# Kernel tuning notes

Measured on AMD Instinct MI355X. Metric: run time of the kernel, lower is better.

Reference implementation:

```python
import jax, jax.numpy as jnp
import numpy as np

B, S, T = 512, 1024, 50


def setup_inputs() -> dict:
    key = jax.random.key(0)
    k1, k2, k3, k4, k5, k6, k7 = jax.random.split(key, 7)
    token_scores = jax.random.normal(k1, (B, S, T), dtype=jnp.float32)
    tags = jax.random.randint(k2, (B, S), 0, T, dtype=jnp.int64)
    # left-contiguous mask: each sequence has a random valid length >= 1
    lengths = jax.random.randint(k3, (B,), 1, S + 1)
    token_mask = (jnp.arange(S)[None, :] < lengths[:, None]).astype(jnp.int32)
    transitions = jax.random.normal(k4, (T, T), dtype=jnp.float32) * 0.1
    start_transitions = jax.random.normal(k5, (T,), dtype=jnp.float32) * 0.1
    end_transitions = jax.random.normal(k6, (T,), dtype=jnp.float32) * 0.1
    return {
        "token_scores": token_scores,
        "tags": tags,
        "token_mask": token_mask,
        "transitions": transitions,
        "start_transitions": start_transitions,
        "end_transitions": end_transitions,
    }


def _crf_log_likelihood(token_scores, tags, token_mask, transitions,
                        start_transitions, end_transitions):
    # token_scores: [B,S,T], tags: [B,S] int, token_mask: [B,S] {0,1}
    maskf = token_mask.astype(token_scores.dtype)
    maskb = token_mask.astype(bool)

    # ---- numerator: score of the gold tag path ----
    emit = jnp.take_along_axis(token_scores, tags[..., None], axis=2)[..., 0]  # [B,S]
    emit_sum = jnp.sum(emit * maskf, axis=1)
    trans_sum = jnp.sum(transitions[tags[:, :-1], tags[:, 1:]] * maskf[:, 1:], axis=1)
    start_score = start_transitions[tags[:, 0]]
    last_idx = jnp.sum(token_mask, axis=1).astype(jnp.int32) - 1          # [B]
    last_tags = jnp.take_along_axis(tags, last_idx[:, None], axis=1)[:, 0]
    end_score = end_transitions[last_tags]
    numerator = start_score + emit_sum + trans_sum + end_score            # [B]

    # ---- denominator: log partition via forward algorithm (scan over time) ----
    alpha0 = start_transitions[None, :] + token_scores[:, 0]              # [B,T]
    logits_rest = jnp.swapaxes(token_scores[:, 1:], 0, 1)                 # [S-1,B,T]
    mask_rest = jnp.swapaxes(maskb[:, 1:], 0, 1)                          # [S-1,B]

    def step(alpha, xs):
        logit_t, m_t = xs                                                 # [B,T], [B]
        # inner[b, i, j] = alpha[b,i] + transitions[i,j] + logit_t[b,j]
        inner = alpha[:, :, None] + transitions[None, :, :] + logit_t[:, None, :]
        new_alpha = jax.nn.logsumexp(inner, axis=1)                       # [B,T]
        alpha = jnp.where(m_t[:, None], new_alpha, alpha)
        return alpha, None

    alpha, _ = jax.lax.scan(step, alpha0, (logits_rest, mask_rest))
    denominator = jax.nn.logsumexp(alpha + end_transitions[None, :], axis=1)  # [B]

    return jnp.sum(numerator - denominator)  # scalar, summed over batch


def reference(token_scores, tags, token_mask, transitions,
              start_transitions, end_transitions):
    batch_size = token_scores.shape[0]
    ll = _crf_log_likelihood(token_scores, tags, token_mask, transitions,
                             start_transitions, end_transitions)
    return -ll / float(batch_size)
```

## Files before the change

kernel.cpp:

```cpp
#include <hip/hip_runtime.h>
#include <math.h>

#define CB 512
#define CS 1024
#define CT 50
#define PF 4

__global__ void zero_out_kernel(float* out) { out[0] = 0.0f; }

__device__ __forceinline__ void wave_fence() {
    __builtin_amdgcn_wave_barrier();
    asm volatile("" ::: "memory");
}

__device__ __forceinline__ int lane0_bits(float v) {
    return __builtin_amdgcn_readlane(__float_as_int(v), 0);
}

__global__ __launch_bounds__(128) void crf_scan_kernel(
    const float* __restrict__ scores,
    const int*   __restrict__ tags,
    const int*   __restrict__ mask,
    const float* __restrict__ trans,
    const float* __restrict__ start_tr,
    const float* __restrict__ end_tr,
    float* __restrict__ out)
{
    const int b    = blockIdx.x;
    const int tid  = threadIdx.x;
    const int w    = tid >> 6;
    const int lane = tid & 63;
    const int xl   = (lane < CT) ? lane : 0;

    __shared__ __attribute__((aligned(16))) float sTrans[CT * CT];
    __shared__ __attribute__((aligned(16))) float sP[2][64];
    __shared__ __attribute__((aligned(16))) float sA[64];
    __shared__ __attribute__((aligned(16))) float sB[64];
    __shared__ float sLZ[2], sN[2];

    for (int k = tid; k < CT * CT; k += 128) sTrans[k] = trans[k];
    __syncthreads();

    float ev[CT];
    #pragma unroll
    for (int i = 0; i < CT; ++i)
        ev[i] = __expf((w == 0) ? sTrans[i * CT + xl] : sTrans[xl * CT + i]);

    const int* mrow = mask + (size_t)b * CS;
    int len = 0;
    for (int t = lane; t < CS; t += 64) len += mrow[t];
    #pragma unroll
    for (int off = 32; off; off >>= 1) len += __shfl_xor(len, off);

    const float* srow = scores + (size_t)b * CS * CT;
    const float* sx   = srow + xl;

    const int tm = (len - 1) >> 1;

    const int count = (w == 0) ? tm : ((len >= 2) ? (len - 2 - tm) : 0);
    const int base  = (w == 0) ? 1 : (len - 2);
    const int dir   = (w == 0) ? 1 : -1;

    float st = (w == 0) ? __expf(start_tr[xl] + sx[0])
                        : ((len >= 2) ? __expf(end_tr[xl] + sx[(size_t)(len - 1) * CT])
                                      : __expf(end_tr[xl]));
    int   kexp = 0;
    float* myP = sP[w];

    #define STEP(EXK)                                                       \
    {                                                                       \
        myP[lane] = st;                                                     \
        wave_fence();                                                       \
        float q0 = 0.f, q1 = 0.f, q2 = 0.f, q3 = 0.f;                       \
        _Pragma("unroll")                                                   \
        for (int i = 0; i < 48; i += 4) {                                   \
            const float4 pv = *(const float4*)&myP[i];                      \
            q0 = fmaf(pv.x, ev[i + 0], q0);                                 \
            q1 = fmaf(pv.y, ev[i + 1], q1);                                 \
            q2 = fmaf(pv.z, ev[i + 2], q2);                                 \
            q3 = fmaf(pv.w, ev[i + 3], q3);                                 \
        }                                                                   \
        {                                                                   \
            const float2 pv2 = *(const float2*)&myP[48];                    \
            q0 = fmaf(pv2.x, ev[48], q0);                                   \
            q1 = fmaf(pv2.y, ev[49], q1);                                   \
        }                                                                   \
        wave_fence();                                                       \
        st = ((q0 + q1) + (q2 + q3)) * (EXK);                               \
    }

    #define RENORM()                                                        \
    {                                                                       \
        int sb = lane0_bits(st);                                            \
        int e  = (sb >> 23) & 0xff;                                         \
        kexp  += e - 127;                                                   \
        st    *= __int_as_float((254 - e) << 23);                           \
    }

    float xpf[PF];
    #pragma unroll
    for (int k = 0; k < PF; ++k) {
        int idx = base + dir * k;
        if (idx < 0) idx = 0;
        xpf[k] = sx[(size_t)idx * CT];
    }
    int k = 0;
    while (k + PF <= count) {
        float exk[PF];
        #pragma unroll
        for (int j = 0; j < PF; ++j) exk[j] = __expf(xpf[j]);
        #pragma unroll
        for (int j = 0; j < PF; ++j) {
            int idx = base + dir * (k + PF + j);
            if (idx < 0) idx = 0;
            xpf[j] = sx[(size_t)idx * CT];
        }
        RENORM();
        STEP(exk[0]); STEP(exk[1]); STEP(exk[2]); STEP(exk[3]);
        k += PF;
    }
    for (int r = 0; k < count; ++k, ++r) {
        float exk = __expf(xpf[r]);
        RENORM();
        STEP(exk);
    }

    if (w == 1 && len >= 2) { STEP(1.0f) }
    RENORM();
    #undef STEP
    #undef RENORM

    if (w == 0) sA[lane] = (lane < CT) ? st : 0.0f;
    else        sB[lane] = (lane < CT) ? st : 0.0f;
    if (lane == 0) sLZ[w] = (float)kexp * 0.6931471805599453f;
    __syncthreads();

    const int* trow = tags + (size_t)b * CS;
    float nsum = 0.0f;
    for (int t = tid; t < CS; t += 128) {
        if (t < len) {
            int tg = trow[t];
            nsum += srow[(size_t)t * CT + tg];
            if (t >= 1) nsum += sTrans[trow[t - 1] * CT + tg];
        }
    }
    #pragma unroll
    for (int off = 32; off; off >>= 1) nsum += __shfl_xor(nsum, off);
    if (lane == 0) sN[w] = nsum;

    float den = 0.0f;
    if (w == 0) {
        float vp = sA[lane] * sB[lane];
        #pragma unroll
        for (int off = 32; off; off >>= 1) vp += __shfl_xor(vp, off);
        den = sLZ[0] + sLZ[1] + __logf(vp);
    }
    __syncthreads();

    if (tid == 0) {
        float num = sN[0] + sN[1] + start_tr[trow[0]] + end_tr[trow[len - 1]];
        atomicAdd(out, (den - num) * (1.0f / CB));
    }
}

extern "C" void kernel_launch(void* const* d_in, const int* in_sizes, int n_in,
                              void* d_out, int out_size, void* d_ws, size_t ws_size,
                              hipStream_t stream) {
    const float* scores   = (const float*)d_in[0];
    const int*   tags     = (const int*)d_in[1];
    const int*   mask     = (const int*)d_in[2];
    const float* trans    = (const float*)d_in[3];
    const float* start_tr = (const float*)d_in[4];
    const float* end_tr   = (const float*)d_in[5];
    float* out = (float*)d_out;

    zero_out_kernel<<<1, 1, 0, stream>>>(out);
    crf_scan_kernel<<<CB, 128, 0, stream>>>(scores, tags, mask, trans,
                                            start_tr, end_tr, out);
}
```

Measured before the change: 293.0 us.

## Split the CRF step matvec across lane quads with packed FMA and DPP reduction

Each recurrence step now has every lane compute partial sums for four output tags over a sixteen-state slice of the input. Each lane reads four float4 values from LDS instead of the whole state vector, and uses packed two-wide FMAs. The quad partials are then combined with DPP quad permutes, and each lane picks its own tag's result. This shortens the serial FMA dependency chain and cuts LDS traffic on the latency-bound sequential scan, at the cost of extra permute and select instructions per step. Launch bounds now also declare one block per SIMD minimum.

```diff
diff --git a/kernel.cpp b/kernel.cpp
--- a/kernel.cpp
+++ b/kernel.cpp
@@ -6,6 +6,8 @@
 #define CT 50
 #define PF 4
 
+typedef float v2f __attribute__((ext_vector_type(2)));
+
 __global__ void zero_out_kernel(float* out) { out[0] = 0.0f; }
 
 __device__ __forceinline__ void wave_fence() {
@@ -17,7 +19,13 @@
     return __builtin_amdgcn_readlane(__float_as_int(v), 0);
 }
 
-__global__ __launch_bounds__(128) void crf_scan_kernel(
+template <int CTRL>
+__device__ __forceinline__ float qperm(float v) {
+    return __int_as_float(__builtin_amdgcn_update_dpp(
+        0, __float_as_int(v), CTRL, 0xf, 0xf, false));
+}
+
+__global__ __launch_bounds__(128, 1) void crf_scan_kernel(
     const float* __restrict__ scores,
     const int*   __restrict__ tags,
     const int*   __restrict__ mask,
@@ -31,9 +39,13 @@
     const int w    = tid >> 6;
     const int lane = tid & 63;
     const int xl   = (lane < CT) ? lane : 0;
+    const int g    = lane & 3;
+    const int m    = lane >> 2;
+    const bool selb0 = (lane & 1) != 0;
+    const bool selb1 = (lane & 2) != 0;
 
     __shared__ __attribute__((aligned(16))) float sTrans[CT * CT];
-    __shared__ __attribute__((aligned(16))) float sP[2][64];
+    __shared__ __attribute__((aligned(16))) float sP2[2][64];
     __shared__ __attribute__((aligned(16))) float sA[64];
     __shared__ __attribute__((aligned(16))) float sB[64];
     __shared__ float sLZ[2], sN[2];
@@ -41,10 +53,26 @@
     for (int k = tid; k < CT * CT; k += 128) sTrans[k] = trans[k];
     __syncthreads();
 
-    float ev[CT];
-    #pragma unroll
-    for (int i = 0; i < CT; ++i)
-        ev[i] = __expf((w == 0) ? sTrans[i * CT + xl] : sTrans[xl * CT + i]);
+    v2f EC0[16], EC1[16];
+    {
+        const int i0 = 16 * g, s0 = 4 * m;
+        #pragma unroll
+        for (int k = 0; k < 16; ++k) {
+            const int i = i0 + k;
+            float e[4] = {0.f, 0.f, 0.f, 0.f};
+            if (i < CT) {
+                #pragma unroll
+                for (int c = 0; c < 4; ++c) {
+                    const int s = s0 + c;
+                    if (s < CT)
+                        e[c] = __expf(w == 0 ? sTrans[i * CT + s]
+                                             : sTrans[s * CT + i]);
+                }
+            }
+            EC0[k] = (v2f){e[0], e[1]};
+            EC1[k] = (v2f){e[2], e[3]};
+        }
+    }
 
     const int* mrow = mask + (size_t)b * CS;
     int len = 0;
@@ -55,38 +83,49 @@
     const float* srow = scores + (size_t)b * CS * CT;
     const float* sx   = srow + xl;
 
-    const int tm = (len - 1) >> 1;
-
+    const int tm    = (len - 1) >> 1;
     const int count = (w == 0) ? tm : ((len >= 2) ? (len - 2 - tm) : 0);
     const int base  = (w == 0) ? 1 : (len - 2);
     const int dir   = (w == 0) ? 1 : -1;
 
-    float st = (w == 0) ? __expf(start_tr[xl] + sx[0])
-                        : ((len >= 2) ? __expf(end_tr[xl] + sx[(size_t)(len - 1) * CT])
-                                      : __expf(end_tr[xl]));
-    int   kexp = 0;
-    float* myP = sP[w];
-
-    #define STEP(EXK)                                                       \
+    float st;
+    if (w == 0) {
+        st = (lane < CT) ? __expf(start_tr[lane] + sx[0]) : 0.f;
+    } else {
+        st = (lane < CT)
+            ? ((len >= 2) ? __expf(end_tr[lane] + sx[(size_t)(len - 1) * CT])
+                          : __expf(end_tr[lane]))
+            : 0.f;
+    }
+    int kexp = 0;
+    float* sP = sP2[w];
+    const float* sPq = sP + 16 * g;
+
+    #define STEP(EX)                                                        \
     {                                                                       \
-        myP[lane] = st;                                                     \
+        sP[lane] = st;                                                      \
         wave_fence();                                                       \
-        float q0 = 0.f, q1 = 0.f, q2 = 0.f, q3 = 0.f;                       \
+        const float4 p0 = *(const float4*)&sPq[0];                          \
+        const float4 p1 = *(const float4*)&sPq[4];                          \
+        const float4 p2 = *(const float4*)&sPq[8];                          \
+        const float4 p3 = *(const float4*)&sPq[12];                         \
+        wave_fence();    \
+        float pv[16] = {p0.x,p0.y,p0.z,p0.w, p1.x,p1.y,p1.z,p1.w,           \
+                        p2.x,p2.y,p2.z,p2.w, p3.x,p3.y,p3.z,p3.w};          \
+        v2f a0 = {0.f,0.f}, a1 = {0.f,0.f};                                 \
         _Pragma("unroll")                                                   \
-        for (int i = 0; i < 48; i += 4) {                                   \
-            const float4 pv = *(const float4*)&myP[i];                      \
-            q0 = fmaf(pv.x, ev[i + 0], q0);                                 \
-            q1 = fmaf(pv.y, ev[i + 1], q1);                                 \
-            q2 = fmaf(pv.z, ev[i + 2], q2);                                 \
-            q3 = fmaf(pv.w, ev[i + 3], q3);                                 \
+        for (int kk = 0; kk < 16; ++kk) {                                   \
+            const v2f t2 = {pv[kk], pv[kk]};                                \
+            a0 = __builtin_elementwise_fma(t2, EC0[kk], a0);                \
+            a1 = __builtin_elementwise_fma(t2, EC1[kk], a1);                \
         }                                                                   \
-        {                                                                   \
-            const float2 pv2 = *(const float2*)&myP[48];                    \
-            q0 = fmaf(pv2.x, ev[48], q0);                                   \
-            q1 = fmaf(pv2.y, ev[49], q1);                                   \
-        }                                                                   \
-        wave_fence();                                                       \
-        st = ((q0 + q1) + (q2 + q3)) * (EXK);                               \
+        a0.x += qperm<0xB1>(a0.x); a0.y += qperm<0xB1>(a0.y);               \
+        a1.x += qperm<0xB1>(a1.x); a1.y += qperm<0xB1>(a1.y);               \
+        a0.x += qperm<0x4E>(a0.x); a0.y += qperm<0x4E>(a0.y);               \
+        a1.x += qperm<0x4E>(a1.x); a1.y += qperm<0x4E>(a1.y);               \
+        const float o01 = selb0 ? a0.y : a0.x;                              \
+        const float o23 = selb0 ? a1.y : a1.x;                              \
+        st = (selb1 ? o23 : o01) * (EX);                                    \
     }
 
     #define RENORM()                                                        \
@@ -120,12 +159,11 @@
         k += PF;
     }
     for (int r = 0; k < count; ++k, ++r) {
-        float exk = __expf(xpf[r]);
+        float e = __expf(xpf[r]);
         RENORM();
-        STEP(exk);
-    }
-
-    if (w == 1 && len >= 2) { STEP(1.0f) }
+        STEP(e);
+    }
+    if (w == 1 && len >= 2) { RENORM(); STEP(1.0f); }
     RENORM();
     #undef STEP
     #undef RENORM
```

Result: faster. 261.6 us (-10.7%).
